# Performance work log

Measured on AMD Instinct MI355X. Metric: run time of the kernel, lower is better.

The kernel has to match this reference:

```python
import jax, jax.numpy as jnp
import numpy as np

BF = 2          # branching_factor
NH = 8          # num_heads
DIM = 64        # dim
PAD = BF + 1    # padding value in path words
N_POS = 2048    # number of positions precomputed


def _pos_to_path(idx, cache):
    if idx in cache:
        return cache[idx]
    parent = (idx - 2) // BF + 1 if idx != 1 else -1
    step = (idx - 2) % BF + 1 if idx != 1 else 0
    cache[idx] = [*_pos_to_path(parent, cache), step]
    return cache[idx]


def setup_inputs() -> dict:
    key = jax.random.key(0)
    # raw parameter: torch.rand -> uniform [0,1)
    primitives_raw = jax.random.uniform(key, (BF * NH + 1, DIM, DIM), dtype=jnp.float32)
    cache = {1: [], 0: [-1], -1: []}
    paths = [_pos_to_path(p, cache) for p in range(N_POS)]
    max_len = max(len(p) for p in paths)
    pw = np.full((N_POS, max_len), PAD, dtype=np.int32)
    for i, p in enumerate(paths):
        pw[i, :len(p)] = p
    return {"primitives_raw": primitives_raw, "path_words": jnp.asarray(pw)}


def reference(primitives_raw, path_words):
    dim = primitives_raw.shape[-1]
    # primitives = expm((A - A^H) / dim); real-valued so mH == transpose
    herm = (primitives_raw - jnp.swapaxes(primitives_raw, -1, -2)) / dim
    prims = jax.vmap(jax.scipy.linalg.expm)(herm)          # [BF*NH+1, d, d]
    sos_repr = prims[-1]                                   # [d, d]
    branch = prims[:-1].reshape(BF, NH, dim, dim)          # [BF, NH, d, d]

    # ---- steps (integer, no grad in original) ----
    point_mask = path_words != PAD                         # [N, L]
    pair_mask = point_mask[:, None, :] & point_mask[None, :, :]
    eqs = (path_words[:, None, :] == path_words[None, :, :]).astype(jnp.int32)
    common_prefix = jnp.cumprod(eqs, axis=-1).astype(bool) & pair_mask
    lens = point_mask.sum(-1)
    max_lens = jnp.maximum(lens[:, None], lens[None, :])
    steps = max_lens - common_prefix.sum(-1)               # [N, N]

    # ---- maps: sequential product of primitives along each path ----
    n = path_words.shape[0]
    eye = jnp.eye(dim, dtype=prims.dtype)
    init = jnp.broadcast_to(eye, (n, NH, dim, dim))
    sos = path_words[:, 0] == -1
    init = jnp.where(sos[:, None, None, None], sos_repr[None, None], init)

    def body(maps, idx_t):
        # Faithful to source: only k in range(BF) matches (value BF acts as identity)
        gate = (idx_t >= 0) & (idx_t < BF)                 # [N]
        mats = jnp.where(gate[:, None, None, None],
                         branch[jnp.clip(idx_t, 0, BF - 1)],  # [N, NH, d, d]
                         eye)
        return jnp.einsum('nhij,nhjk->nhik', maps, mats), None

    maps, _ = jax.lax.scan(body, init, path_words.T)       # scan over depth L
    return maps, steps
```

## Files before the change

### kernel.cpp

```cpp
#include <hip/hip_runtime.h>

#define DIM 64
#define NHEADS 8
#define NPOS 2048
#define PADW 3

typedef float f32x4 __attribute__((ext_vector_type(4)));

#define C1 1.0f
#define C2 0.5f
#define C3 (1.0f / 6.0f)
#define C4 (1.0f / 24.0f)
#define C5 (1.0f / 120.0f)
#define C6 (1.0f / 720.0f)
#define C7 (1.0f / 5040.0f)
#define C8 (1.0f / 40320.0f)

__device__ __forceinline__ f32x4 ld4(const float* p) { return *reinterpret_cast<const f32x4*>(p); }
__device__ __forceinline__ void st4(float* p, f32x4 v) { *reinterpret_cast<f32x4*>(p) = v; }
__device__ __forceinline__ void tzero(float (&a)[4][4]) {
#pragma unroll
  for (int i = 0; i < 4; ++i)
#pragma unroll
    for (int j = 0; j < 4; ++j) a[i][j] = 0.0f;
}
__device__ __forceinline__ void tfma(float (&a)[4][4], const f32x4 x, const f32x4 y) {
#pragma unroll
  for (int i = 0; i < 4; ++i)
#pragma unroll
    for (int j = 0; j < 4; ++j) a[i][j] = fmaf(x[i], y[j], a[i][j]);
}

__global__ __launch_bounds__(256, 1) void prologue_kernel(const float* __restrict__ U,
                                                          float* __restrict__ powers) {
  __shared__ __align__(16) float b0[4096];
  __shared__ __align__(16) float b1[4096];
  __shared__ __align__(16) float b2[4096];
  __shared__ __align__(16) float b3[4096];
  const int t = threadIdx.x;
  const int b = blockIdx.x;
  const bool sos = (b == 88);
  const int kp = sos ? 1 : (b >> 3);
  float* __restrict__ dst = powers + (size_t)b * 4096;

  if (kp == 0) {
    for (int i = t; i < 4096; i += 256) dst[i] = ((i >> 6) == (i & 63)) ? 1.0f : 0.0f;
    return;
  }

  const int m = sos ? 16 : (NHEADS + (b & 7));
  const float* __restrict__ Um = U + (size_t)m * 4096;
  const float scale = (float)kp * (1.0f / 256.0f);

  const int r0 = ((t >> 4) & 15) << 2;
  const int c0 = (t & 15) << 2;

  {
    f32x4 ur[4], uc[4];
#pragma unroll
    for (int i = 0; i < 4; ++i) ur[i] = ld4(&Um[(r0 + i) * 64 + c0]);
#pragma unroll
    for (int j = 0; j < 4; ++j) uc[j] = ld4(&Um[(c0 + j) * 64 + r0]);
#pragma unroll
    for (int i = 0; i < 4; ++i) {
      f32x4 v;
#pragma unroll
      for (int j = 0; j < 4; ++j) v[j] = scale * (ur[i][j] - uc[j][i]);
      st4(&b0[(r0 + i) * 64 + c0], v);
    }
  }
  __syncthreads();

  {
    float a[4][4];
    tzero(a);
#pragma unroll 4
    for (int k = 0; k < 64; ++k) tfma(a, ld4(&b0[k * 64 + r0]), ld4(&b0[k * 64 + c0]));
#pragma unroll
    for (int i = 0; i < 4; ++i) {
      f32x4 v;
#pragma unroll
      for (int j = 0; j < 4; ++j) v[j] = -a[i][j];
      st4(&b1[(r0 + i) * 64 + c0], v);
    }
  }
  __syncthreads();

  {
    float a3[4][4], a4[4][4];
    tzero(a3);
    tzero(a4);
#pragma unroll 4
    for (int k = 0; k < 64; ++k) {
      const f32x4 msr = ld4(&b0[k * 64 + r0]);
      const f32x4 m2r = ld4(&b1[k * 64 + r0]);
      const f32x4 m2c = ld4(&b1[k * 64 + c0]);
      tfma(a3, msr, m2c);
      tfma(a4, m2r, m2c);
    }
#pragma unroll
    for (int i = 0; i < 4; ++i) {
      f32x4 v3, v4;
#pragma unroll
      for (int j = 0; j < 4; ++j) {
        v3[j] = -a3[i][j];
        v4[j] = a4[i][j];
      }
      st4(&b2[(r0 + i) * 64 + c0], v3);
      st4(&b3[(r0 + i) * 64 + c0], v4);
    }
  }
  __syncthreads();

  {
    float aE[4][4], aO[4][4];
    tzero(aE);
    tzero(aO);
#pragma unroll 2
    for (int k = 0; k < 64; ++k) {
      const f32x4 xv = ld4(&b3[k * 64 + r0]);
      const f32x4 msv = ld4(&b0[k * 64 + c0]);
      const f32x4 m2v = ld4(&b1[k * 64 + c0]);
      const f32x4 m3v = ld4(&b2[k * 64 + c0]);
      const f32x4 m4v = ld4(&b3[k * 64 + c0]);
      f32x4 ev, ov, yv, yw;
#pragma unroll
      for (int j = 0; j < 4; ++j) {
        ev[j] = fmaf(C8, m4v[j], C6 * m2v[j]);
        ov[j] = fmaf(C7, m3v[j], C5 * msv[j]);
        yv[j] = ev[j] + ov[j];
        yw[j] = ev[j] - ov[j];
      }
      tfma(aE, xv, yv);
      tfma(aO, xv, yw);
    }
    float eT[4][4], oT[4][4];
#pragma unroll
    for (int i = 0; i < 4; ++i) {
      const f32x4 msr = ld4(&b0[(r0 + i) * 64 + c0]);
      const f32x4 m2r = ld4(&b1[(r0 + i) * 64 + c0]);
      const f32x4 m3r = ld4(&b2[(r0 + i) * 64 + c0]);
      const f32x4 m4r = ld4(&b3[(r0 + i) * 64 + c0]);
#pragma unroll
      for (int j = 0; j < 4; ++j) {
        const float d = (r0 + i == c0 + j) ? 1.0f : 0.0f;
        const float even = d + fmaf(C4, m4r[j], C2 * m2r[j]);
        const float odd = fmaf(C3, m3r[j], C1 * msr[j]);
        eT[i][j] = aE[i][j] + even + odd;
        oT[i][j] = aO[i][j] + even - odd;
      }
    }
    __syncthreads();
#pragma unroll
    for (int i = 0; i < 4; ++i) {
      f32x4 ve, vo;
#pragma unroll
      for (int j = 0; j < 4; ++j) {
        ve[j] = eT[i][j];
        vo[j] = oT[i][j];
      }
      st4(&b0[(r0 + i) * 64 + c0], ve);
      st4(&b1[(r0 + i) * 64 + c0], vo);
    }
  }
  __syncthreads();

  {
    float aA[4][4], aB[4][4];
    tzero(aA);
    tzero(aB);
#pragma unroll 2
    for (int k = 0; k < 64; ++k) {
      const f32x4 etr = ld4(&b1[k * 64 + r0]);
      const f32x4 er = ld4(&b0[k * 64 + r0]);
      const f32x4 ec = ld4(&b0[k * 64 + c0]);
      const f32x4 etc2 = ld4(&b1[k * 64 + c0]);
      tfma(aA, etr, ec);
      tfma(aB, er, etc2);
    }
#pragma unroll
    for (int i = 0; i < 4; ++i) {
      f32x4 va, vb;
#pragma unroll
      for (int j = 0; j < 4; ++j) {
        va[j] = aA[i][j];
        vb[j] = aB[i][j];
      }
      st4(&b2[(r0 + i) * 64 + c0], va);
      st4(&b3[(r0 + i) * 64 + c0], vb);
    }
  }
  __syncthreads();

  {
    float a[4][4];
    tzero(a);
#pragma unroll 4
    for (int k = 0; k < 64; ++k) tfma(a, ld4(&b3[k * 64 + r0]), ld4(&b2[k * 64 + c0]));
#pragma unroll
    for (int i = 0; i < 4; ++i) {
      f32x4 v;
#pragma unroll
      for (int j = 0; j < 4; ++j) v[j] = a[i][j];
      st4(&dst[(r0 + i) * 64 + c0], v);
    }
  }
}

__global__ __launch_bounds__(256) void outputs_kernel(const float* __restrict__ powers,
                                                      const int* __restrict__ pw, int L,
                                                      float* __restrict__ out_maps,
                                                      float* __restrict__ out_steps) {
  const int t = threadIdx.x;
  if (blockIdx.x < NPOS) {
    const int n = blockIdx.x;
    const int* row = pw + (size_t)n * L;
    const bool sos = (row[0] == -1);
    int c = 0;
    for (int s = 0; s < L; ++s) {
      const int w = row[s];
      c += (w >= 0 && w < 2) ? 1 : 0;
    }
#pragma unroll
    for (int h = 0; h < NHEADS; ++h) {
      const float* src = sos ? (powers + (size_t)88 * 4096)
                             : (powers + (size_t)(c * NHEADS + h) * 4096);
      const f32x4* s4 = reinterpret_cast<const f32x4*>(src);
      f32x4* d4 = reinterpret_cast<f32x4*>(out_maps + ((size_t)n * NHEADS + h) * 4096);
#pragma unroll
      for (int i = 0; i < 4; ++i) {
        const f32x4 v = s4[t + 256 * i];
        __builtin_nontemporal_store(v, &d4[t + 256 * i]);
      }
    }
  } else {
    const int tb = blockIdx.x - NPOS;
    const int bi = (tb >> 6) * 32, bj = (tb & 63) * 32;
    __shared__ int pwi[32][16];
    __shared__ int pwj[32][16];
    __shared__ int li[32], lj[32];
    if (t < 32) {
      const int* row = pw + (size_t)(bi + t) * L;
      int len = 0;
      for (int s = 0; s < L; ++s) {
        const int w = row[s];
        pwi[t][s] = w;
        len += (w != PADW);
      }
      li[t] = len;
    } else if (t < 64) {
      const int r = t - 32;
      const int* row = pw + (size_t)(bj + r) * L;
      int len = 0;
      for (int s = 0; s < L; ++s) {
        const int w = row[s];
        pwj[r][s] = w;
        len += (w != PADW);
      }
      lj[r] = len;
    }
    __syncthreads();
    const int tx = t & 31, ty0 = t >> 5;
#pragma unroll
    for (int m = 0; m < 4; ++m) {
      const int ty = ty0 + 8 * m;
      int prefix = 1, common = 0;
      for (int s = 0; s < L; ++s) {
        const int wi = pwi[ty][s], wj = pwj[tx][s];
        prefix &= (wi == wj);
        common += prefix & (int)(wi != PADW) & (int)(wj != PADW);
      }
      const float steps = (float)(max(li[ty], lj[tx]) - common);
      __builtin_nontemporal_store(steps, &out_steps[(size_t)(bi + ty) * NPOS + (bj + tx)]);
    }
  }
}

extern "C" void kernel_launch(void* const* d_in, const int* in_sizes, int n_in,
                              void* d_out, int out_size, void* d_ws, size_t ws_size,
                              hipStream_t stream) {
  const float* U = (const float*)d_in[0];
  const int* pw = (const int*)d_in[1];
  const int L = in_sizes[1] / NPOS;

  float* powers = (float*)d_ws;

  float* out_maps = (float*)d_out;
  float* out_steps = out_maps + (size_t)NPOS * NHEADS * 4096;

  hipLaunchKernelGGL(prologue_kernel, dim3(89), dim3(256), 0, stream, U, powers);
  hipLaunchKernelGGL(outputs_kernel, dim3(NPOS + 64 * 64), dim3(256), 0, stream,
                     powers, pw, L, out_maps, out_steps);
}
```

Before: 315.0 us.

## Pack path words into bitmasks and compute common prefix via ctz; reorder blocks

Each path row is packed into a 64-bit word with 3 bits per symbol, and the common prefix length becomes the count of trailing zeros of the XOR divided by 3, replacing the per-symbol loop. The steps blocks now come before the map-copy blocks in the grid, and the nontemporal stores are swapped for ordinary stores. The intent is to cut ALU and LDS work on the steps side and change scheduling and cache behaviour on the store-bound copy. Packing assumes L is at most 21 and that every symbol plus one fits in 3 bits.

```diff
diff --git a/kernel.cpp b/kernel.cpp
--- a/kernel.cpp
+++ b/kernel.cpp
@@ -212,8 +212,45 @@
                                                       float* __restrict__ out_maps,
                                                       float* __restrict__ out_steps) {
   const int t = threadIdx.x;
-  if (blockIdx.x < NPOS) {
-    const int n = blockIdx.x;
+  if (blockIdx.x < 64 * 64) {
+    const int tb = blockIdx.x;
+    const int bi = (tb >> 6) * 32, bj = (tb & 63) * 32;
+    __shared__ unsigned long long pki[32], pkj[32];
+    __shared__ int li[32], lj[32];
+    if (t < 64) {
+      const int r = (t < 32) ? (bi + t) : (bj + (t - 32));
+      const int* row = pw + (size_t)r * L;
+      int len = 0;
+      unsigned long long packed = 0ull;
+      for (int s = 0; s < L; ++s) {
+        const int w = row[s];
+        len += (w != PADW) ? 1 : 0;
+        packed |= (unsigned long long)(unsigned)(w + 1) << (3 * s);
+      }
+      if (t < 32) {
+        pki[t] = packed;
+        li[t] = len;
+      } else {
+        pkj[t - 32] = packed;
+        lj[t - 32] = len;
+      }
+    }
+    __syncthreads();
+    const int tx = t & 31, ty0 = t >> 5;
+    const unsigned long long xj = pkj[tx];
+    const int lenj = lj[tx];
+#pragma unroll
+    for (int m = 0; m < 4; ++m) {
+      const int ty = ty0 + 8 * m;
+      const unsigned long long x = pki[ty] ^ xj;
+      const int leni = li[ty];
+      const int p = x ? (__builtin_ctzll(x) / 3) : L;
+      const int common = min(p, min(leni, lenj));
+      const float steps = (float)(max(leni, lenj) - common);
+      out_steps[(size_t)(bi + ty) * NPOS + (bj + tx)] = steps;
+    }
+  } else {
+    const int n = blockIdx.x - 64 * 64;
     const int* row = pw + (size_t)n * L;
     const bool sos = (row[0] == -1);
     int c = 0;
@@ -228,50 +265,7 @@
       const f32x4* s4 = reinterpret_cast<const f32x4*>(src);
       f32x4* d4 = reinterpret_cast<f32x4*>(out_maps + ((size_t)n * NHEADS + h) * 4096);
 #pragma unroll
-      for (int i = 0; i < 4; ++i) {
-        const f32x4 v = s4[t + 256 * i];
-        __builtin_nontemporal_store(v, &d4[t + 256 * i]);
-      }
-    }
-  } else {
-    const int tb = blockIdx.x - NPOS;
-    const int bi = (tb >> 6) * 32, bj = (tb & 63) * 32;
-    __shared__ int pwi[32][16];
-    __shared__ int pwj[32][16];
-    __shared__ int li[32], lj[32];
-    if (t < 32) {
-      const int* row = pw + (size_t)(bi + t) * L;
-      int len = 0;
-      for (int s = 0; s < L; ++s) {
-        const int w = row[s];
-        pwi[t][s] = w;
-        len += (w != PADW);
-      }
-      li[t] = len;
-    } else if (t < 64) {
-      const int r = t - 32;
-      const int* row = pw + (size_t)(bj + r) * L;
-      int len = 0;
-      for (int s = 0; s < L; ++s) {
-        const int w = row[s];
-        pwj[r][s] = w;
-        len += (w != PADW);
-      }
-      lj[r] = len;
-    }
-    __syncthreads();
-    const int tx = t & 31, ty0 = t >> 5;
-#pragma unroll
-    for (int m = 0; m < 4; ++m) {
-      const int ty = ty0 + 8 * m;
-      int prefix = 1, common = 0;
-      for (int s = 0; s < L; ++s) {
-        const int wi = pwi[ty][s], wj = pwj[tx][s];
-        prefix &= (wi == wj);
-        common += prefix & (int)(wi != PADW) & (int)(wj != PADW);
-      }
-      const float steps = (float)(max(li[ty], lj[tx]) - common);
-      __builtin_nontemporal_store(steps, &out_steps[(size_t)(bi + ty) * NPOS + (bj + tx)]);
+      for (int i = 0; i < 4; ++i) d4[t + 256 * i] = s4[t + 256 * i];
     }
   }
 }
@@ -289,6 +283,6 @@
   float* out_steps = out_maps + (size_t)NPOS * NHEADS * 4096;
 
   hipLaunchKernelGGL(prologue_kernel, dim3(89), dim3(256), 0, stream, U, powers);
-  hipLaunchKernelGGL(outputs_kernel, dim3(NPOS + 64 * 64), dim3(256), 0, stream,
+  hipLaunchKernelGGL(outputs_kernel, dim3(64 * 64 + NPOS), dim3(256), 0, stream,
                      powers, pw, L, out_maps, out_steps);
 }
```

Result: faster. 298.2 us (-5.3%).
